# Kernel tuning notes

Measured on AMD Instinct MI355X. Metric: run time of the kernel, lower is better.

## Reference

```python
import jax, jax.numpy as jnp
import numpy as np

C = 512
H_HEADS = 8  # self-attn heads (num_heads) and cross-attn heads (n_heads), both 8


def _self_attn(x, Wq, Wkv):
    # x: [B,N,C]; shared (ModuleParallel) linear weights, qkv_bias=False
    B, N, _ = x.shape
    h, d = H_HEADS, C // H_HEADS
    q = (x @ Wq.T).reshape(B, N, h, d).transpose(0, 2, 1, 3)          # [B,h,N,d]
    kv = (x @ Wkv.T).reshape(B, N, 2, h, d).transpose(2, 0, 3, 1, 4)  # [2,B,h,N,d]
    k, v = kv[0], kv[1]
    attn = jax.nn.softmax(jnp.einsum('bhnd,bhmd->bhnm', q, k) * (d ** -0.5), axis=-1)
    y = jnp.einsum('bhnm,bhmd->bhnd', attn, v).transpose(0, 2, 1, 3).reshape(B, N, C)
    return y


def _judger(y_self, y_other, Wj1, bj1, Wj2, bj2):
    # Mlp_2(2C->C->C) with exact GELU, then softmax over channel dim
    hdn = jax.nn.gelu(jnp.concatenate([y_self, y_other], axis=-1) @ Wj1.T + bj1, approximate=False)
    return jax.nn.softmax(hdn @ Wj2.T + bj2, axis=-1)


def _cross_attn(yq, ykv, kn_row, vn_row, Win, bin_, Wout, bout, rel):
    # Vectorized form of the per-sample loop: each token is a seq-len-1 query
    # attending over 2 keys: [noise_k + yq, yq * relation_score].
    B, N, _ = yq.shape
    h, d = H_HEADS, C // H_HEADS
    qw, kw, vw = Win[:C], Win[C:2 * C], Win[2 * C:]
    bq, bk, bv = bin_[:C], bin_[C:2 * C], bin_[2 * C:]
    k_in = jnp.stack([kn_row + yq, yq * rel], axis=-2)   # [B,N,2,C]
    v_in = jnp.stack([vn_row + yq, ykv], axis=-2)        # [B,N,2,C]
    qp = (yq @ qw.T + bq).reshape(B, N, h, d)
    kp = (k_in @ kw.T + bk).reshape(B, N, 2, h, d)
    vp = (v_in @ vw.T + bv).reshape(B, N, 2, h, d)
    scores = jnp.einsum('bnhd,bnkhd->bnhk', qp, kp) * (d ** -0.5)
    w = jax.nn.softmax(scores, axis=-1)
    o = jnp.einsum('bnhk,bnkhd->bnhd', w, vp).reshape(B, N, C)
    return o @ Wout.T + bout


def setup_inputs() -> dict:
    key = jax.random.key(0)
    ks = jax.random.split(key, 16)
    B, N = 8, 1024
    s = 0.02
    inp = {
        'x0': jax.random.normal(ks[0], (B, N, C), jnp.float32),
        'x1': jax.random.normal(ks[1], (B, N, C), jnp.float32),
        'H': 32, 'W': 32,
        'Wq': jax.random.normal(ks[2], (C, C), jnp.float32) * s,
        'Wkv': jax.random.normal(ks[3], (2 * C, C), jnp.float32) * s,
        'Wj1': jax.random.normal(ks[4], (C, 2 * C), jnp.float32) * s,
        'bj1': jnp.zeros((C,), jnp.float32),
        'Wj2': jax.random.normal(ks[5], (C, C), jnp.float32) * s,
        'bj2': jnp.zeros((C,), jnp.float32),
        'kn': jax.random.normal(ks[6], (2, C), jnp.float32),
        'vn': jax.random.normal(ks[7], (2, C), jnp.float32),
        'Wc0_in': jax.random.normal(ks[8], (3 * C, C), jnp.float32) * s,
        'bc0_in': jnp.zeros((3 * C,), jnp.float32),
        'Wc0_out': jax.random.normal(ks[9], (C, C), jnp.float32) * s,
        'bc0_out': jnp.zeros((C,), jnp.float32),
        'Wc1_in': jax.random.normal(ks[10], (3 * C, C), jnp.float32) * s,
        'bc1_in': jnp.zeros((3 * C,), jnp.float32),
        'Wc1_out': jax.random.normal(ks[11], (C, C), jnp.float32) * s,
        'bc1_out': jnp.zeros((C,), jnp.float32),
        'Wp': jax.random.normal(ks[12], (C, C), jnp.float32) * s,
        'bp': jnp.zeros((C,), jnp.float32),
    }
    return inp


def reference(x0, x1, H, W, Wq, Wkv, Wj1, bj1, Wj2, bj2, kn, vn,
              Wc0_in, bc0_in, Wc0_out, bc0_out, Wc1_in, bc1_in, Wc1_out, bc1_out,
              Wp, bp):
    # Dual self-attention (shared q/kv projections across modalities, sr_ratio=1)
    y0 = _self_attn(x0, Wq, Wkv)
    y1 = _self_attn(x1, Wq, Wkv)
    # Noise-augmented relation-gated cross-attention (vectorized over batch)
    rel0 = _judger(y0, y1, Wj1, bj1, Wj2, bj2)
    rel1 = _judger(y1, y0, Wj1, bj1, Wj2, bj2)
    new0 = y0 + _cross_attn(y0, y1, kn[0], vn[0], Wc0_in, bc0_in, Wc0_out, bc0_out, rel0)
    new1 = y1 + _cross_attn(y1, y0, kn[1], vn[1], Wc1_in, bc1_in, Wc1_out, bc1_out, rel1)
    out0 = new0 @ Wp.T + bp
    out1 = new1 @ Wp.T + bp
    return jnp.stack([out0, out1])  # [2,B,N,C]
```

## Files before the change

kernel.cpp:

```cpp
#include <hip/hip_runtime.h>

typedef unsigned short u16;
typedef u16 u16x8 __attribute__((ext_vector_type(8)));
typedef __bf16 bf16x8 __attribute__((ext_vector_type(8)));
typedef __bf16 bf16x2 __attribute__((ext_vector_type(2)));
typedef float f32x4 __attribute__((ext_vector_type(4)));

__device__ __forceinline__ float b2f(u16 h) {
  union { unsigned u; float f; } x; x.u = ((unsigned)h) << 16; return x.f;
}
__device__ __forceinline__ u16 f2b(float f) {
  union { float f; unsigned u; } x; x.f = f;
  unsigned r = x.u + 0x7FFFu + ((x.u >> 16) & 1u);
  return (u16)(r >> 16);
}
__device__ __forceinline__ f32x4 mfma16(bf16x8 a, bf16x8 b, f32x4 c) {
  return __builtin_amdgcn_mfma_f32_16x16x32_bf16(a, b, c, 0, 0, 0);
}
__device__ __forceinline__ void gload16(const void* g, void* l) {
  __builtin_amdgcn_global_load_lds(
      (const __attribute__((address_space(1))) void*)g,
      (__attribute__((address_space(3))) void*)l, 16, 0, 0);
}
#define WAITV8 asm volatile("s_waitcnt vmcnt(8)" ::: "memory")
#define WAITV4 asm volatile("s_waitcnt vmcnt(4)" ::: "memory")
#define WAITV0 asm volatile("s_waitcnt vmcnt(0)" ::: "memory")
#define WAITL0 asm volatile("s_waitcnt lgkmcnt(0)" ::: "memory")
#define BARRIER asm volatile("s_barrier" ::: "memory")

__global__ __launch_bounds__(256) void xcvt_k(const float* __restrict__ x0,
                                              const float* __restrict__ x1,
                                              u16* __restrict__ out) {
  int b = blockIdx.x;
  const float* src = (b < 4096) ? x0 : x1;
  u16* dst = out + (b < 4096 ? 0 : 4194304);
  int i = (b & 4095) * 1024 + threadIdx.x * 4;
  float4 v = *(const float4*)&src[i];
  dst[i + 0] = f2b(v.x); dst[i + 1] = f2b(v.y);
  dst[i + 2] = f2b(v.z); dst[i + 3] = f2b(v.w);
}

__global__ __launch_bounds__(256) void wcvt_k(
    const float* __restrict__ wq, const float* __restrict__ wkv,
    const float* __restrict__ wj1, const float* __restrict__ wj2,
    const float* __restrict__ wci0, const float* __restrict__ wci1,
    const float* __restrict__ wp, u16* __restrict__ wsb) {
  int b = blockIdx.x; const float* src; size_t doff; int lb;
  if      (b < 256)  { src = wq;   doff = 0;       lb = b; }
  else if (b < 768)  { src = wkv;  doff = 262144;  lb = b - 256; }
  else if (b < 1280) { src = wj1;  doff = 786432;  lb = b - 768; }
  else if (b < 1536) { src = wj2;  doff = 1310720; lb = b - 1280; }
  else if (b < 2304) { src = wci0; doff = 1572864; lb = b - 1536; }
  else if (b < 3072) { src = wci1; doff = 2359296; lb = b - 2304; }
  else               { src = wp;   doff = 3145728; lb = b - 3072; }
  int i = lb * 1024 + threadIdx.x * 4;
  float4 v = *(const float4*)&src[i];
  u16* dst = wsb + doff + i;
  u16 c0 = f2b(v.x), c1 = f2b(v.y), c2 = f2b(v.z), c3 = f2b(v.w);
  dst[0] = c0; dst[1] = c1; dst[2] = c2; dst[3] = c3;
  if (b >= 3072) {
    int row = i >> 9, col = i & 511;
    u16* f0 = wsb + 3932160 + (size_t)row * 1024 + col;
    u16* f1 = wsb + 4456448 + (size_t)row * 1024 + col;
    f0[0] = c0; f0[1] = c1; f0[2] = c2; f0[3] = c3;
    f1[0] = c0; f1[1] = c1; f1[2] = c2; f1[3] = c3;
  }
}

__global__ __launch_bounds__(256) void tcvt_k(const float* __restrict__ w0,
                                              const float* __restrict__ w1,
                                              u16* __restrict__ o0,
                                              u16* __restrict__ o1) {
  __shared__ u16 t[64][65];
  const int b = blockIdx.x;
  const float* src = (b & 64) ? w1 : w0;
  u16* dst = (b & 64) ? o1 : o0;
  const int r0 = ((b >> 3) & 7) * 64, c0 = (b & 7) * 64;
  const int tid = threadIdx.x;
#pragma unroll
  for (int i = 0; i < 16; i++) {
    int idx = tid + i * 256;
    int r = idx >> 6, c = idx & 63;
    t[r][c] = f2b(src[(size_t)(r0 + r) * 512 + c0 + c]);
  }
  __syncthreads();
#pragma unroll
  for (int i = 0; i < 16; i++) {
    int idx = tid + i * 256;
    int c = idx >> 6, r = idx & 63;
    dst[(size_t)(c0 + c) * 512 + r0 + r] = t[r][c];
  }
}

__global__ __launch_bounds__(256) void cvec_k(
    const float* __restrict__ kn, const float* __restrict__ vn,
    const float* __restrict__ bp, const float* __restrict__ bco0,
    const float* __restrict__ bco1, const u16* __restrict__ wci0,
    const u16* __restrict__ wci1, const u16* __restrict__ wp,
    float* __restrict__ out) {
  int idx = blockIdx.x * 256 + threadIdx.x;
  int which = idx >> 9, col = idx & 511;
  const float* src; const u16* w; float acc;
  if (which < 4) {
    int s = which & 1, isv = which >> 1;
    src = (isv ? vn : kn) + s * 512;
    w = (s ? wci1 : wci0) + (isv ? 524288 : 262144) + (size_t)col * 512;
    acc = 0.f;
  } else {
    int s = which & 1;
    src = s ? bco1 : bco0;
    w = wp + (size_t)col * 512;
    acc = bp[col];
  }
  for (int k = 0; k < 512; k += 8) {
    u16x8 w8 = *(const u16x8*)&w[k];
#pragma unroll
    for (int j = 0; j < 8; j++) acc += src[k + j] * b2f(w8[j]);
  }
  out[idx] = acc;
}

template<int EPI, int AMODE>
__global__ __launch_bounds__(256, 3) void gemm6_k(
    const u16* __restrict__ A, int astr, int K1, int K,
    const u16* __restrict__ W0, const u16* __restrict__ W1,
    const float* __restrict__ b0, const float* __restrict__ b1,
    void* __restrict__ outp, int ostr, int ncol) {
  __shared__ u16 SM[32768];
  const int tid = threadIdx.x, lane = tid & 63, wv = tid >> 6;
  const int wr = wv >> 1, wc = wv & 1;
  const int lr = lane & 15, lg = lane >> 4;
  const int L = blockIdx.x;
  const int nrow = gridDim.x / ncol;
  int row_b, col_b;
  if ((nrow & 7) == 0) {
    int xcd = L & 7, s = L >> 3;
    row_b = xcd * (nrow >> 3) + s / ncol;
    col_b = s % ncol;
  } else { row_b = L % nrow; col_b = L / nrow; }
  const int row0 = row_b * 128, col0 = col_b * 128;
  const int strm = (row0 >= 8192) ? 1 : 0;
  const u16* W = strm ? W1 : W0;
  const float* bias = strm ? b1 : b0;
  const int shift = (AMODE == 4 && col0 >= 1536) ? 512 : 0;
  const int cxor  = (AMODE == 4 && col0 >= 1536) ? 8192 : 0;
  const int bcl = (lane & 7) * 16;

  f32x4 acc[4][4];
#pragma unroll
  for (int m = 0; m < 4; m++)
#pragma unroll
    for (int n = 0; n < 4; n++) acc[m][n] = f32x4{0.f, 0.f, 0.f, 0.f};

  const int nk = K >> 6;

  auto stage = [&](int k0, int buf) {
    const int Ab = buf * 16384, Wb = buf * 16384 + 8192;
#pragma unroll
    for (int ch = 0; ch < 4; ch++) {
      int r = ch * 32 + (tid >> 3);
      int bcs = bcl ^ ((r & 7) << 4);
      const char* asrc;
      if constexpr (AMODE == 3) {
        if (k0 < K1)
          asrc = (const char*)(A + (size_t)(row0 + r) * astr) + k0 * 2 + bcs;
        else
          asrc = (const char*)(A + (size_t)((row0 + r) ^ 8192) * astr) +
                 (k0 - K1) * 2 + bcs;
      } else {
        asrc = (const char*)(A + (size_t)((row0 + r) ^ cxor) * astr) +
               k0 * 2 + bcs;
      }
      gload16(asrc, &SM[Ab + (ch * 32 + wv * 8) * 64]);
      const char* wsrc =
          (const char*)(W + (size_t)(col0 - shift + r) * K) + k0 * 2 + bcs;
      gload16(wsrc, &SM[Wb + (ch * 32 + wv * 8) * 64]);
    }
  };

  stage(0, 0);
  for (int t = 0; t < nk; t++) {
    const int buf = t & 1;
    if (t + 1 < nk) {
      stage((t + 1) * 64, buf ^ 1);
      WAITV8;
    } else {
      WAITV0;
    }
    BARRIER;
    const int Ab = buf * 16384, Wb = buf * 16384 + 8192;
#pragma unroll
    for (int kk = 0; kk < 2; kk++) {
      const int c = kk * 32 + lg * 8;
      bf16x8 af[4], wf[4];
#pragma unroll
      for (int m = 0; m < 4; m++) {
        int r = wr * 64 + m * 16 + lr;
        af[m] = *(const bf16x8*)&SM[Ab + r * 64 + (c ^ ((r & 7) << 3))];
      }
#pragma unroll
      for (int n = 0; n < 4; n++) {
        int r = wc * 64 + n * 16 + lr;
        wf[n] = *(const bf16x8*)&SM[Wb + r * 64 + (c ^ ((r & 7) << 3))];
      }
#pragma unroll
      for (int m = 0; m < 4; m++)
#pragma unroll
        for (int n = 0; n < 4; n++)
          acc[m][n] = mfma16(af[m], wf[n], acc[m][n]);
    }
    WAITL0;
    BARRIER;
  }

#pragma unroll
  for (int m = 0; m < 4; m++)
#pragma unroll
    for (int n = 0; n < 4; n++)
#pragma unroll
      for (int r = 0; r < 4; r++) {
        int grow = row0 + wr * 64 + m * 16 + lg * 4 + r;
        int gcol = col0 + wc * 64 + n * 16 + lr;
        float v = acc[m][n][r];
        if (bias) v += bias[gcol - shift];
        if (EPI == 1) v = 0.5f * v * (1.0f + erff(v * 0.70710678118f));
        if (EPI == 3) ((float*)outp)[(size_t)grow * ostr + gcol] = v;
        else          ((u16*)outp)[(size_t)grow * ostr + gcol] = f2b(v);
      }
}

__global__ __launch_bounds__(256) void vtrans_k(const u16* __restrict__ QKV,
                                                u16* __restrict__ VT) {
  __shared__ u16 t[64][66];
  const int tid = threadIdx.x;
  const int bh = blockIdx.y;
  const int sb = bh >> 3, h = bh & 7;
  const int n0 = blockIdx.x * 64;
#pragma unroll
  for (int i = 0; i < 16; i++) {
    int idx = tid + i * 256;
    int r = idx >> 6, c = idx & 63;
    t[r][c] = QKV[((size_t)sb * 1024 + n0 + r) * 1536 + 1024 + h * 64 + c];
  }
  __syncthreads();
#pragma unroll
  for (int i = 0; i < 16; i++) {
    int idx = tid + i * 256;
    int r = idx >> 6, p = idx & 63;
    int tok = ((p >> 5) << 5) + ((p & 31) >> 1) + ((p & 1) << 4);
    VT[((size_t)bh * 64 + r) * 1024 + n0 + p] = t[tok][r];
  }
}

__global__ __launch_bounds__(256) void attn_k(const u16* __restrict__ QKV,
                                              const u16* __restrict__ VT,
                                              u16* __restrict__ OC) {
  __shared__ u16 SM[24576];
  const int STR = 1536;
  const int tid = threadIdx.x, lane = tid & 63, wv = tid >> 6;
  const int lr = lane & 15, lg = lane >> 4;
  const int L = blockIdx.x;
  const int by = L & 127;
  const int q0 = (L >> 7) * 128;
  const int sb = by >> 3, h = by & 7;
  const size_t rowbase = (size_t)sb * 1024;
  const int bcl = (lane & 7) * 16;
  const float SC = 0.18033688f;

  bf16x8 qa[2][2];
#pragma unroll
  for (int m = 0; m < 2; m++)
#pragma unroll
    for (int kk = 0; kk < 2; kk++) {
      int r = q0 + wv * 32 + m * 16 + lr;
      int c = h * 64 + kk * 32 + lg * 8;
      qa[m][kk] = *(const bf16x8*)&QKV[(rowbase + r) * STR + c];
    }

  f32x4 o[2][4];
#pragma unroll
  for (int m = 0; m < 2; m++)
#pragma unroll
    for (int n = 0; n < 4; n++) o[m][n] = f32x4{0.f, 0.f, 0.f, 0.f};
  float ls[2][4] = {{0.f, 0.f, 0.f, 0.f}, {0.f, 0.f, 0.f, 0.f}};

  auto stagekv = [&](int c0, int buf) {
#pragma unroll
    for (int ch = 0; ch < 2; ch++) {
      int r = ch * 32 + (tid >> 3);
      int bcs = bcl ^ ((r & 7) << 4);
      const char* ks =
          (const char*)(QKV + (rowbase + c0 + r) * STR + 512 + h * 64) + bcs;
      gload16(ks, &SM[buf * 8192 + (ch * 32 + wv * 8) * 64]);
      const char* vs =
          (const char*)(VT + ((size_t)by * 64 + r) * 1024 + c0) + bcs;
      gload16(vs, &SM[buf * 8192 + 4096 + (ch * 32 + wv * 8) * 64]);
    }
  };

  stagekv(0, 0);
  for (int t = 0; t < 16; t++) {
    const int buf = t & 1;
    if (t < 15) {
      stagekv((t + 1) * 64, buf ^ 1);
      WAITV4;
    } else {
      WAITV0;
    }
    BARRIER;
    const int Kb = buf * 8192, Vb = buf * 8192 + 4096;

    f32x4 s[2][4];
#pragma unroll
    for (int m = 0; m < 2; m++)
#pragma unroll
      for (int n = 0; n < 4; n++) s[m][n] = f32x4{0.f, 0.f, 0.f, 0.f};
#pragma unroll
    for (int kk = 0; kk < 2; kk++) {
      const int c = kk * 32 + lg * 8;
      bf16x8 kf[4];
#pragma unroll
      for (int n = 0; n < 4; n++) {
        int r = n * 16 + lr;
        kf[n] = *(const bf16x8*)&SM[Kb + r * 64 + (c ^ ((r & 7) << 3))];
      }
#pragma unroll
      for (int m = 0; m < 2; m++)
#pragma unroll
        for (int n = 0; n < 4; n++) s[m][n] = mfma16(qa[m][kk], kf[n], s[m][n]);
    }
#pragma unroll
    for (int m = 0; m < 2; m++)
#pragma unroll
      for (int r = 0; r < 4; r++) {
        int prow = wv * 32 + m * 16 + lg * 4 + r;
        float p00 = __builtin_amdgcn_exp2f(s[m][0][r] * SC);
        float p01 = __builtin_amdgcn_exp2f(s[m][1][r] * SC);
        float p10 = __builtin_amdgcn_exp2f(s[m][2][r] * SC);
        float p11 = __builtin_amdgcn_exp2f(s[m][3][r] * SC);
        ls[m][r] += (p00 + p01) + (p10 + p11);
        bf16x2 w0; w0[0] = (__bf16)p00; w0[1] = (__bf16)p01;
        bf16x2 w1; w1[0] = (__bf16)p10; w1[1] = (__bf16)p11;
        int ib = 16384 + prow * 64, xr = (prow & 7) << 3;
        *(bf16x2*)&SM[ib + ((lr * 2) ^ xr)] = w0;
        *(bf16x2*)&SM[ib + ((32 + lr * 2) ^ xr)] = w1;
      }
#pragma unroll
    for (int kc = 0; kc < 2; kc++) {
      const int cc = kc * 32 + lg * 8;
      bf16x8 pa[2], vf[4];
#pragma unroll
      for (int m = 0; m < 2; m++) {
        int r = wv * 32 + m * 16 + lr;
        pa[m] = *(const bf16x8*)&SM[16384 + r * 64 + (cc ^ ((r & 7) << 3))];
      }
#pragma unroll
      for (int n = 0; n < 4; n++) {
        int r = n * 16 + lr;
        vf[n] = *(const bf16x8*)&SM[Vb + r * 64 + (cc ^ ((r & 7) << 3))];
      }
#pragma unroll
      for (int m = 0; m < 2; m++)
#pragma unroll
        for (int n = 0; n < 4; n++) o[m][n] = mfma16(pa[m], vf[n], o[m][n]);
    }
    WAITL0;
    BARRIER;
  }

#pragma unroll
  for (int m = 0; m < 2; m++)
#pragma unroll
    for (int r = 0; r < 4; r++) {
      float v = ls[m][r];
      v += __shfl_xor(v, 1); v += __shfl_xor(v, 2);
      v += __shfl_xor(v, 4); v += __shfl_xor(v, 8);
      ls[m][r] = v;
    }
#pragma unroll
  for (int m = 0; m < 2; m++)
#pragma unroll
    for (int n = 0; n < 4; n++)
#pragma unroll
      for (int r = 0; r < 4; r++) {
        int grow = q0 + wv * 32 + m * 16 + lg * 4 + r;
        int gcol = h * 64 + n * 16 + lr;
        OC[(rowbase + grow) * 1024 + gcol] = f2b(o[m][n][r] / ls[m][r]);
      }
}

__global__ __launch_bounds__(256) void relmul_k(const u16* __restrict__ RL,
                                                const u16* __restrict__ OC,
                                                u16* __restrict__ YKR) {
  const int row = blockIdx.x * 4 + (threadIdx.x >> 6);
  const int lane = threadIdx.x & 63;
  u16x8 lv = *(const u16x8*)&RL[(size_t)row * 512 + lane * 8];
  float e[8]; float s = 0.f;
#pragma unroll
  for (int j = 0; j < 8; j++) { e[j] = __expf(b2f(lv[j])); s += e[j]; }
  for (int x = 1; x < 64; x <<= 1) s += __shfl_xor(s, x);
  float inv = 1.0f / s;
  u16x8 y8 = *(const u16x8*)&OC[(size_t)row * 1024 + lane * 8];
  u16x8 o8;
#pragma unroll
  for (int j = 0; j < 8; j++) o8[j] = f2b(b2f(y8[j]) * (e[j] * inv));
  *(u16x8*)&YKR[(size_t)row * 512 + lane * 8] = o8;
}

__global__ __launch_bounds__(256) void twokey3_k(const u16* __restrict__ CP,
                                                 const u16* __restrict__ KP1,
                                                 const float* __restrict__ cvec,
                                                 u16* __restrict__ OC) {
  const int t = blockIdx.x * 4 + (threadIdx.x >> 6);
  const int lane = threadIdx.x & 63;
  const int s = t >> 13;
  const size_t rb = (size_t)t * 2048 + lane * 8;
  u16x8 q8 = *(const u16x8*)&CP[rb];
  u16x8 a8 = *(const u16x8*)&CP[rb + 512];
  u16x8 v0 = *(const u16x8*)&CP[rb + 1024];
  u16x8 v1 = *(const u16x8*)&CP[rb + 1536];
  u16x8 b8 = *(const u16x8*)&KP1[(size_t)t * 512 + lane * 8];
  const float* ck = cvec + s * 512 + lane * 8;
  const float* cv = cvec + 1024 + s * 512 + lane * 8;

  float s0 = 0.f, s1 = 0.f;
#pragma unroll
  for (int j = 0; j < 8; j++) {
    float qf = b2f(q8[j]);
    s0 += qf * (b2f(a8[j]) + ck[j]);
    s1 += qf * b2f(b8[j]);
  }
  s0 += __shfl_xor(s0, 1); s1 += __shfl_xor(s1, 1);
  s0 += __shfl_xor(s0, 2); s1 += __shfl_xor(s1, 2);
  s0 += __shfl_xor(s0, 4); s1 += __shfl_xor(s1, 4);

  float e0 = __expf(s0 * 0.125f), e1 = __expf(s1 * 0.125f);
  float rr = 1.0f / (e0 + e1);
  float w0 = e0 * rr, w1 = e1 * rr;
  u16x8 o8;
#pragma unroll
  for (int j = 0; j < 8; j++)
    o8[j] = f2b(w0 * (b2f(v0[j]) + cv[j]) + w1 * b2f(v1[j]));
  *(u16x8*)&OC[(size_t)t * 1024 + 512 + lane * 8] = o8;
}

extern "C" void kernel_launch(void* const* d_in, const int* in_sizes, int n_in,
                              void* d_out, int out_size, void* d_ws, size_t ws_size,
                              hipStream_t stream) {
  (void)in_sizes; (void)n_in; (void)out_size; (void)ws_size;
  const float* x0  = (const float*)d_in[0];
  const float* x1  = (const float*)d_in[1];
  const float* Wq  = (const float*)d_in[4];
  const float* Wkv = (const float*)d_in[5];
  const float* Wj1 = (const float*)d_in[6];
  const float* bj1 = (const float*)d_in[7];
  const float* Wj2 = (const float*)d_in[8];
  const float* bj2 = (const float*)d_in[9];
  const float* kn  = (const float*)d_in[10];
  const float* vn  = (const float*)d_in[11];
  const float* Wci[2]  = {(const float*)d_in[12], (const float*)d_in[16]};
  const float* bci[2]  = {(const float*)d_in[13], (const float*)d_in[17]};
  const float* Wco[2]  = {(const float*)d_in[14], (const float*)d_in[18]};
  const float* bco[2]  = {(const float*)d_in[15], (const float*)d_in[19]};
  const float* Wp  = (const float*)d_in[20];
  const float* bp  = (const float*)d_in[21];

  u16* wsb = (u16*)d_ws;
  u16* wqb   = wsb;
  u16* wj1b  = wsb + 786432;
  u16* wj2b  = wsb + 1310720;
  u16* wcib[2] = {wsb + 1572864, wsb + 2359296};
  u16* wpb   = wsb + 3145728;
  u16* wcoT[2] = {wsb + 3407872, wsb + 3670016};
  u16* wfin[2] = {wsb + 3932160, wsb + 4456448};
  float* cvecb = (float*)(wsb + 4980736);
  const size_t SLOT = 8388608;
  u16* base = wsb + 5242880;
  u16* S0 = base;
  u16* OC = base + 1 * SLOT;
  u16* S3 = base + 3 * SLOT;
  u16* S4 = base + 4 * SLOT;
  u16* S6 = base + 6 * SLOT;
  u16* QKV = S3;
  u16* REL = S3;
  u16* CP  = S3;
  u16* YKR = S4;

  dim3 blk(256);
  xcvt_k<<<dim3(8192), blk, 0, stream>>>(x0, x1, S0);
  wcvt_k<<<dim3(3328), blk, 0, stream>>>(Wq, Wkv, Wj1, Wj2, Wci[0], Wci[1],
                                         Wp, wsb);
  tcvt_k<<<dim3(128), blk, 0, stream>>>(Wco[0], Wco[1], wcoT[0], wcoT[1]);
  cvec_k<<<dim3(12), blk, 0, stream>>>(kn, vn, bp, bco[0], bco[1],
                                       wcib[0], wcib[1], wpb, cvecb);
  for (int s = 0; s < 2; s++)
    gemm6_k<0, 0><<<dim3(16), blk, 0, stream>>>(
        wpb, 512, 512, 512, wcoT[s], wcoT[s], nullptr, nullptr,
        wfin[s] + 512, 1024, 4);

  gemm6_k<0, 0><<<dim3(1536), blk, 0, stream>>>(
      S0, 512, 512, 512, wqb, wqb, nullptr, nullptr, QKV, 1536, 12);
  vtrans_k<<<dim3(16, 128), blk, 0, stream>>>(QKV, S6);
  attn_k<<<dim3(1024), blk, 0, stream>>>(QKV, S6, OC);

  gemm6_k<1, 3><<<dim3(512), blk, 0, stream>>>(
      OC, 1024, 512, 1024, wj1b, wj1b, bj1, bj1, S0, 512, 4);
  gemm6_k<0, 0><<<dim3(512), blk, 0, stream>>>(
      S0, 512, 512, 512, wj2b, wj2b, bj2, bj2, REL, 512, 4);
  relmul_k<<<dim3(4096), blk, 0, stream>>>(REL, OC, YKR);
  gemm6_k<0, 0><<<dim3(512), blk, 0, stream>>>(
      YKR, 512, 512, 512, wcib[0] + 262144, wcib[1] + 262144,
      bci[0] + 512, bci[1] + 512, S0, 512, 4);
  gemm6_k<0, 4><<<dim3(2048), blk, 0, stream>>>(
      OC, 1024, 512, 512, wcib[0], wcib[1], bci[0], bci[1], CP, 2048, 16);

  twokey3_k<<<dim3(4096), blk, 0, stream>>>(CP, S0, cvecb, OC);

  gemm6_k<3, 0><<<dim3(512), blk, 0, stream>>>(
      OC, 1024, 1024, 1024, wfin[0], wfin[1], cvecb + 2048, cvecb + 2560,
      d_out, 512, 4);
}
```

Baseline: 347.6 us.

## Use 512-thread GEMM blocks and drop LDS staging of K/V in attention

The GEMM now runs 8 waves per 128x128 tile instead of 4, so each wave owns a 32x64 sub-tile with half the accumulators. Staging uses 2 chunks per thread and the wait count is lowered to match, aiming at more waves in flight per CU. Separately, the attention kernel no longer double-buffers K and V through LDS and reads MFMA fragments straight from global memory, keeping only the P tile in shared memory. That removes barriers and LDS traffic but exposes global load latency and repeated, less coalesced reads in the attention inner loop.

```diff
diff --git a/kernel.cpp b/kernel.cpp
--- a/kernel.cpp
+++ b/kernel.cpp
@@ -22,7 +22,6 @@
       (const __attribute__((address_space(1))) void*)g,
       (__attribute__((address_space(3))) void*)l, 16, 0, 0);
 }
-#define WAITV8 asm volatile("s_waitcnt vmcnt(8)" ::: "memory")
 #define WAITV4 asm volatile("s_waitcnt vmcnt(4)" ::: "memory")
 #define WAITV0 asm volatile("s_waitcnt vmcnt(0)" ::: "memory")
 #define WAITL0 asm volatile("s_waitcnt lgkmcnt(0)" ::: "memory")
@@ -121,13 +120,15 @@
 }
 
 template<int EPI, int AMODE>
-__global__ __launch_bounds__(256, 3) void gemm6_k(
+__global__ __launch_bounds__(512, 4) void gemm9_k(
     const u16* __restrict__ A, int astr, int K1, int K,
     const u16* __restrict__ W0, const u16* __restrict__ W1,
     const float* __restrict__ b0, const float* __restrict__ b1,
     void* __restrict__ outp, int ostr, int ncol) {
   __shared__ u16 SM[32768];
-  const int tid = threadIdx.x, lane = tid & 63, wv = tid >> 6;
+  const int tid = threadIdx.x;
+  const int lane = tid & 63;
+  const int wv = tid >> 6;
   const int wr = wv >> 1, wc = wv & 1;
   const int lr = lane & 15, lg = lane >> 4;
   const int L = blockIdx.x;
@@ -144,11 +145,12 @@
   const float* bias = strm ? b1 : b0;
   const int shift = (AMODE == 4 && col0 >= 1536) ? 512 : 0;
   const int cxor  = (AMODE == 4 && col0 >= 1536) ? 8192 : 0;
+  const int rL = tid >> 3;
   const int bcl = (lane & 7) * 16;
 
-  f32x4 acc[4][4];
-#pragma unroll
-  for (int m = 0; m < 4; m++)
+  f32x4 acc[2][4];
+#pragma unroll
+  for (int m = 0; m < 2; m++)
 #pragma unroll
     for (int n = 0; n < 4; n++) acc[m][n] = f32x4{0.f, 0.f, 0.f, 0.f};
 
@@ -157,8 +159,8 @@
   auto stage = [&](int k0, int buf) {
     const int Ab = buf * 16384, Wb = buf * 16384 + 8192;
 #pragma unroll
-    for (int ch = 0; ch < 4; ch++) {
-      int r = ch * 32 + (tid >> 3);
+    for (int ch = 0; ch < 2; ch++) {
+      int r = ch * 64 + rL;
       int bcs = bcl ^ ((r & 7) << 4);
       const char* asrc;
       if constexpr (AMODE == 3) {
@@ -171,10 +173,10 @@
         asrc = (const char*)(A + (size_t)((row0 + r) ^ cxor) * astr) +
                k0 * 2 + bcs;
       }
-      gload16(asrc, &SM[Ab + (ch * 32 + wv * 8) * 64]);
+      gload16(asrc, &SM[Ab + (ch * 64 + wv * 8) * 64]);
       const char* wsrc =
           (const char*)(W + (size_t)(col0 - shift + r) * K) + k0 * 2 + bcs;
-      gload16(wsrc, &SM[Wb + (ch * 32 + wv * 8) * 64]);
+      gload16(wsrc, &SM[Wb + (ch * 64 + wv * 8) * 64]);
     }
   };
 
@@ -183,7 +185,7 @@
     const int buf = t & 1;
     if (t + 1 < nk) {
       stage((t + 1) * 64, buf ^ 1);
-      WAITV8;
+      WAITV4;
     } else {
       WAITV0;
     }
@@ -192,10 +194,10 @@
 #pragma unroll
     for (int kk = 0; kk < 2; kk++) {
       const int c = kk * 32 + lg * 8;
-      bf16x8 af[4], wf[4];
-#pragma unroll
-      for (int m = 0; m < 4; m++) {
-        int r = wr * 64 + m * 16 + lr;
+      bf16x8 af[2], wf[4];
+#pragma unroll
+      for (int m = 0; m < 2; m++) {
+        int r = wr * 32 + m * 16 + lr;
         af[m] = *(const bf16x8*)&SM[Ab + r * 64 + (c ^ ((r & 7) << 3))];
       }
 #pragma unroll
@@ -204,7 +206,7 @@
         wf[n] = *(const bf16x8*)&SM[Wb + r * 64 + (c ^ ((r & 7) << 3))];
       }
 #pragma unroll
-      for (int m = 0; m < 4; m++)
+      for (int m = 0; m < 2; m++)
 #pragma unroll
         for (int n = 0; n < 4; n++)
           acc[m][n] = mfma16(af[m], wf[n], acc[m][n]);
@@ -214,12 +216,12 @@
   }
 
 #pragma unroll
-  for (int m = 0; m < 4; m++)
+  for (int m = 0; m < 2; m++)
 #pragma unroll
     for (int n = 0; n < 4; n++)
 #pragma unroll
       for (int r = 0; r < 4; r++) {
-        int grow = row0 + wr * 64 + m * 16 + lg * 4 + r;
+        int grow = row0 + wr * 32 + m * 16 + lg * 4 + r;
         int gcol = col0 + wc * 64 + n * 16 + lr;
         float v = acc[m][n][r];
         if (bias) v += bias[gcol - shift];
@@ -255,7 +257,7 @@
 __global__ __launch_bounds__(256) void attn_k(const u16* __restrict__ QKV,
                                               const u16* __restrict__ VT,
                                               u16* __restrict__ OC) {
-  __shared__ u16 SM[24576];
+  __shared__ u16 Pt[128 * 64];
   const int STR = 1536;
   const int tid = threadIdx.x, lane = tid & 63, wv = tid >> 6;
   const int lr = lane & 15, lg = lane >> 4;
@@ -264,7 +266,6 @@
   const int q0 = (L >> 7) * 128;
   const int sb = by >> 3, h = by & 7;
   const size_t rowbase = (size_t)sb * 1024;
-  const int bcl = (lane & 7) * 16;
   const float SC = 0.18033688f;
 
   bf16x8 qa[2][2];
@@ -284,32 +285,8 @@
     for (int n = 0; n < 4; n++) o[m][n] = f32x4{0.f, 0.f, 0.f, 0.f};
   float ls[2][4] = {{0.f, 0.f, 0.f, 0.f}, {0.f, 0.f, 0.f, 0.f}};
 
-  auto stagekv = [&](int c0, int buf) {
-#pragma unroll
-    for (int ch = 0; ch < 2; ch++) {
-      int r = ch * 32 + (tid >> 3);
-      int bcs = bcl ^ ((r & 7) << 4);
-      const char* ks =
-          (const char*)(QKV + (rowbase + c0 + r) * STR + 512 + h * 64) + bcs;
-      gload16(ks, &SM[buf * 8192 + (ch * 32 + wv * 8) * 64]);
-      const char* vs =
-          (const char*)(VT + ((size_t)by * 64 + r) * 1024 + c0) + bcs;
-      gload16(vs, &SM[buf * 8192 + 4096 + (ch * 32 + wv * 8) * 64]);
-    }
-  };
-
-  stagekv(0, 0);
   for (int t = 0; t < 16; t++) {
-    const int buf = t & 1;
-    if (t < 15) {
-      stagekv((t + 1) * 64, buf ^ 1);
-      WAITV4;
-    } else {
-      WAITV0;
-    }
-    BARRIER;
-    const int Kb = buf * 8192, Vb = buf * 8192 + 4096;
-
+    const int c0 = t * 64;
     f32x4 s[2][4];
 #pragma unroll
     for (int m = 0; m < 2; m++)
@@ -321,8 +298,8 @@
       bf16x8 kf[4];
 #pragma unroll
       for (int n = 0; n < 4; n++) {
-        int r = n * 16 + lr;
-        kf[n] = *(const bf16x8*)&SM[Kb + r * 64 + (c ^ ((r & 7) << 3))];
+        kf[n] = *(const bf16x8*)&QKV[(rowbase + c0 + n * 16 + lr) * STR +
+                                     512 + h * 64 + c];
       }
 #pragma unroll
       for (int m = 0; m < 2; m++)
@@ -341,9 +318,9 @@
         ls[m][r] += (p00 + p01) + (p10 + p11);
         bf16x2 w0; w0[0] = (__bf16)p00; w0[1] = (__bf16)p01;
         bf16x2 w1; w1[0] = (__bf16)p10; w1[1] = (__bf16)p11;
-        int ib = 16384 + prow * 64, xr = (prow & 7) << 3;
-        *(bf16x2*)&SM[ib + ((lr * 2) ^ xr)] = w0;
-        *(bf16x2*)&SM[ib + ((32 + lr * 2) ^ xr)] = w1;
+        int ib = prow * 64, xr = (prow & 7) << 3;
+        *(bf16x2*)&Pt[ib + ((lr * 2) ^ xr)] = w0;
+        *(bf16x2*)&Pt[ib + ((32 + lr * 2) ^ xr)] = w1;
       }
 #pragma unroll
     for (int kc = 0; kc < 2; kc++) {
@@ -352,20 +329,18 @@
 #pragma unroll
       for (int m = 0; m < 2; m++) {
         int r = wv * 32 + m * 16 + lr;
-        pa[m] = *(const bf16x8*)&SM[16384 + r * 64 + (cc ^ ((r & 7) << 3))];
+        pa[m] = *(const bf16x8*)&Pt[r * 64 + (cc ^ ((r & 7) << 3))];
       }
 #pragma unroll
       for (int n = 0; n < 4; n++) {
-        int r = n * 16 + lr;
-        vf[n] = *(const bf16x8*)&SM[Vb + r * 64 + (cc ^ ((r & 7) << 3))];
+        vf[n] = *(const bf16x8*)&VT[((size_t)by * 64 + n * 16 + lr) * 1024 +
+                                    c0 + cc];
       }
 #pragma unroll
       for (int m = 0; m < 2; m++)
 #pragma unroll
         for (int n = 0; n < 4; n++) o[m][n] = mfma16(pa[m], vf[n], o[m][n]);
     }
-    WAITL0;
-    BARRIER;
   }
 
 #pragma unroll
@@ -486,7 +461,7 @@
   u16* CP  = S3;
   u16* YKR = S4;
 
-  dim3 blk(256);
+  dim3 blk(256), gblk(512);
   xcvt_k<<<dim3(8192), blk, 0, stream>>>(x0, x1, S0);
   wcvt_k<<<dim3(3328), blk, 0, stream>>>(Wq, Wkv, Wj1, Wj2, Wci[0], Wci[1],
                                          Wp, wsb);
@@ -494,29 +469,29 @@
   cvec_k<<<dim3(12), blk, 0, stream>>>(kn, vn, bp, bco[0], bco[1],
                                        wcib[0], wcib[1], wpb, cvecb);
   for (int s = 0; s < 2; s++)
-    gemm6_k<0, 0><<<dim3(16), blk, 0, stream>>>(
+    gemm9_k<0, 0><<<dim3(16), gblk, 0, stream>>>(
         wpb, 512, 512, 512, wcoT[s], wcoT[s], nullptr, nullptr,
         wfin[s] + 512, 1024, 4);
 
-  gemm6_k<0, 0><<<dim3(1536), blk, 0, stream>>>(
+  gemm9_k<0, 0><<<dim3(1536), gblk, 0, stream>>>(
       S0, 512, 512, 512, wqb, wqb, nullptr, nullptr, QKV, 1536, 12);
   vtrans_k<<<dim3(16, 128), blk, 0, stream>>>(QKV, S6);
   attn_k<<<dim3(1024), blk, 0, stream>>>(QKV, S6, OC);
 
-  gemm6_k<1, 3><<<dim3(512), blk, 0, stream>>>(
+  gemm9_k<1, 3><<<dim3(512), gblk, 0, stream>>>(
       OC, 1024, 512, 1024, wj1b, wj1b, bj1, bj1, S0, 512, 4);
-  gemm6_k<0, 0><<<dim3(512), blk, 0, stream>>>(
+  gemm9_k<0, 0><<<dim3(512), gblk, 0, stream>>>(
       S0, 512, 512, 512, wj2b, wj2b, bj2, bj2, REL, 512, 4);
   relmul_k<<<dim3(4096), blk, 0, stream>>>(REL, OC, YKR);
-  gemm6_k<0, 0><<<dim3(512), blk, 0, stream>>>(
+  gemm9_k<0, 0><<<dim3(512), gblk, 0, stream>>>(
       YKR, 512, 512, 512, wcib[0] + 262144, wcib[1] + 262144,
       bci[0] + 512, bci[1] + 512, S0, 512, 4);
-  gemm6_k<0, 4><<<dim3(2048), blk, 0, stream>>>(
+  gemm9_k<0, 4><<<dim3(2048), gblk, 0, stream>>>(
       OC, 1024, 512, 512, wcib[0], wcib[1], bci[0], bci[1], CP, 2048, 16);
 
   twokey3_k<<<dim3(4096), blk, 0, stream>>>(CP, S0, cvecb, OC);
 
-  gemm6_k<3, 0><<<dim3(512), blk, 0, stream>>>(
+  gemm9_k<3, 0><<<dim3(512), gblk, 0, stream>>>(
       OC, 1024, 1024, 1024, wfin[0], wfin[1], cvecb + 2048, cvecb + 2560,
       d_out, 512, 4);
 }
```

Result: slower. 384.2 us (+10.5%).
